# Kernel tuning notes

Hardware: AMD Instinct MI355X
Metric: run time of the kernel (lower is better)

Reference implementation:

```python
import jax, jax.numpy as jnp
import numpy as np

N = 50000          # nodes
E = 800000         # edges (avg degree 16)
FEAT = 128         # self.feat_dim
MAX_SPK = 3
SPK_DIM = 16
SPA_DIM = 16
OUT = 64


def _lin(key, din, dout):
    kw, kb = jax.random.split(key)
    w = jax.random.normal(kw, (din, dout), dtype=jnp.float32) * (1.0 / np.sqrt(din))
    b = jax.random.normal(kb, (dout,), dtype=jnp.float32) * 0.01
    return w, b


def setup_inputs() -> dict:
    key = jax.random.key(0)
    ks = jax.random.split(key, 16)
    D = 7 * FEAT + 5  # 901
    x = jax.random.normal(ks[0], (N, D), dtype=jnp.float32)
    # last column is a speaker count in {1..4} (clamped to max 3 in forward)
    num_spk = jax.random.randint(ks[1], (N,), 1, 5).astype(jnp.float32)
    x = x.at[:, -1].set(num_spk)
    edge_index = jax.random.randint(ks[2], (2, E), 0, N, dtype=jnp.int32)
    edge_attr = jnp.zeros((E,), dtype=jnp.int32)  # all pass the (==111)|(==0) filter

    speaker_w, speaker_b = _lin(ks[3], MAX_SPK, SPK_DIM)
    spatial_w, spatial_b = _lin(ks[4], 4, SPA_DIM)
    # face_trans params
    f1_w, f1_b = _lin(ks[5], FEAT, OUT)
    f2_w, f2_b = _lin(ks[6], FEAT + SPK_DIM + SPA_DIM, OUT)
    fe_w, fe_b = _lin(ks[7], 2 * OUT, 2)
    # face_body_trans params
    g1_w, g1_b = _lin(ks[8], FEAT, OUT)
    g2_w, g2_b = _lin(ks[9], FEAT + SPK_DIM + SPA_DIM, OUT)
    ge_w, ge_b = _lin(ks[10], 2 * OUT, 2)
    return dict(x=x, edge_index=edge_index, edge_attr=edge_attr,
                speaker_w=speaker_w, speaker_b=speaker_b,
                spatial_w=spatial_w, spatial_b=spatial_b,
                f1_w=f1_w, f1_b=f1_b, f2_w=f2_w, f2_b=f2_b, fe_w=fe_w, fe_b=fe_b,
                g1_w=g1_w, g1_b=g1_b, g2_w=g2_w, g2_b=g2_b, ge_w=ge_w, ge_b=ge_b)


def _edge_conv(h, src, dst, valid, ew, eb):
    # PyG EdgeConv (aggr='max'): out_i = max_j MLP([x_i, x_j - x_i])
    hi = h[dst]                                   # [E, 64]
    hj = h[src]                                   # [E, 64]
    msg = jnp.concatenate([hi, hj - hi], axis=1) @ ew + eb  # [E, 2]
    msg = jnp.where(valid[:, None], msg, -jnp.inf)
    out = jax.ops.segment_max(msg, dst, num_segments=h.shape[0])
    return jnp.where(jnp.isfinite(out), out, 0.0)  # empty segments -> 0 (PyG fill)


def reference(x, edge_index, edge_attr,
              speaker_w, speaker_b, spatial_w, spatial_b,
              f1_w, f1_b, f2_w, f2_b, fe_w, fe_b,
              g1_w, g1_b, g2_w, g2_b, ge_w, ge_b):
    valid = (edge_attr == 111) | (edge_attr == 0)
    src, dst = edge_index[0], edge_index[1]

    # speaker-count embedding: one_hot(clamp(x[:,-1]-1, max=2)) -> Linear(3,16)
    spk_idx = jnp.minimum(x[:, -1] - 1.0, MAX_SPK - 1).astype(jnp.int32)
    spk = jax.nn.one_hot(spk_idx, MAX_SPK, dtype=x.dtype) @ speaker_w + speaker_b
    spa = x[:, -5:-1] @ spatial_w + spatial_b

    def block(feat, fc1_w, fc1_b, fc2_w, fc2_b, ew, eb):
        # dropout p=0.9 is identity in eval mode
        h = (feat @ fc1_w + fc1_b) + (jnp.concatenate([feat, spk, spa], axis=1) @ fc2_w + fc2_b)
        return _edge_conv(h, src, dst, valid, ew, eb)

    o_face = block(x[:, :FEAT], f1_w, f1_b, f2_w, f2_b, fe_w, fe_b)
    o_body = block(x[:, FEAT:2 * FEAT], g1_w, g1_b, g2_w, g2_b, ge_w, ge_b)
    return o_face + o_body
```

## Files before the change

kernel.cpp:

```cpp
#include <hip/hip_runtime.h>
#include <hip/hip_bf16.h>
#include <math.h>

#define ROWLEN 901
#define NEGENC 0x007FFFFFu

__device__ __forceinline__ unsigned encf(float f) {
    unsigned u = __float_as_uint(f);
    return (u & 0x80000000u) ? ~u : (u | 0x80000000u);
}
__device__ __forceinline__ float decf(unsigned u) {
    return (u & 0x80000000u) ? __uint_as_float(u ^ 0x80000000u)
                             : __uint_as_float(~u);
}

__global__ __launch_bounds__(256) void k_compose(
    const float* __restrict__ spkw, const float* __restrict__ spkb,
    const float* __restrict__ spaw, const float* __restrict__ spab,
    const float* __restrict__ f1w, const float* __restrict__ f1b,
    const float* __restrict__ f2w, const float* __restrict__ f2b,
    const float* __restrict__ few, const float* __restrict__ feb,
    const float* __restrict__ g1w, const float* __restrict__ g1b,
    const float* __restrict__ g2w, const float* __restrict__ g2b,
    const float* __restrict__ gew, const float* __restrict__ geb,
    float* __restrict__ C, float* __restrict__ Sp,
    float* __restrict__ Tab, float* __restrict__ Cst)
{
    const int t = threadIdx.x;
    __shared__ float sEW[2][256];
    __shared__ float sUV[2][2][2][16][2];
    __shared__ float sBE[8][8];

    sEW[0][t] = few[t];
    sEW[1][t] = gew[t];
    __syncthreads();

    {
        const int blk = t >> 7;
        const int fr  = t & 127;
        const float* w1 = blk ? g1w : f1w;
        const float* w2 = blk ? g2w : f2w;
        const float* e  = sEW[blk];
        float a0 = 0.f, a1 = 0.f, a2 = 0.f, a3 = 0.f;
        #pragma unroll
        for (int k4 = 0; k4 < 16; ++k4) {
            const float4 wa = *(const float4*)(w1 + fr * 64 + k4 * 4);
            const float4 wb = *(const float4*)(w2 + fr * 64 + k4 * 4);
            const float wv[4] = {wa.x + wb.x, wa.y + wb.y, wa.z + wb.z, wa.w + wb.w};
            #pragma unroll
            for (int j = 0; j < 4; ++j) {
                const int k = k4 * 4 + j;
                const float eb0 = e[(64 + k) * 2 + 0];
                const float eb1 = e[(64 + k) * 2 + 1];
                const float ea0 = e[k * 2 + 0] - eb0;
                const float ea1 = e[k * 2 + 1] - eb1;
                a0 += wv[j] * ea0; a1 += wv[j] * ea1;
                a2 += wv[j] * eb0; a3 += wv[j] * eb1;
            }
        }
        C[t * 4 + 0] = a0; C[t * 4 + 1] = a1;
        C[t * 4 + 2] = a2; C[t * 4 + 3] = a3;
    }

    {
        const int c    = t & 1;
        const int k16  = (t >> 1) & 15;
        const int role = (t >> 5) & 1;
        const int blk  = (t >> 6) & 1;
        const int isV  = (t >> 7) & 1;
        const float* w2 = blk ? g2w : f2w;
        const float* e  = sEW[blk];
        const int row = (isV ? 144 : 128) + k16;
        float acc = 0.f;
        #pragma unroll
        for (int k4 = 0; k4 < 16; ++k4) {
            const float4 w = *(const float4*)(w2 + row * 64 + k4 * 4);
            const float wv[4] = {w.x, w.y, w.z, w.w};
            #pragma unroll
            for (int j = 0; j < 4; ++j) {
                const int k = k4 * 4 + j;
                const float ev = role ? e[(64 + k) * 2 + c]
                                      : (e[k * 2 + c] - e[(64 + k) * 2 + c]);
                acc += wv[j] * ev;
            }
        }
        sUV[isV][blk][role][k16][c] = acc;
    }

    if (t < 64) {
        const int combo = t >> 3;
        const int part  = t & 7;
        const int c = combo & 1, role = (combo >> 1) & 1, blk = combo >> 2;
        const float* b1 = blk ? g1b : f1b;
        const float* b2 = blk ? g2b : f2b;
        const float* e  = sEW[blk];
        float acc = 0.f;
        #pragma unroll
        for (int j = 0; j < 8; ++j) {
            const int k = part * 8 + j;
            const float ev = role ? e[(64 + k) * 2 + c]
                                  : (e[k * 2 + c] - e[(64 + k) * 2 + c]);
            acc += (b1[k] + b2[k]) * ev;
        }
        sBE[combo][part] = acc;
    }
    __syncthreads();

    if (t < 24) {
        const int blk = t / 12, rem = t % 12;
        const int idx = rem >> 2, q = rem & 3;
        const int role = q >> 1, c = q & 1;
        float acc = 0.f;
        #pragma unroll
        for (int k = 0; k < 16; ++k)
            acc += spkw[idx * 16 + k] * sUV[0][blk][role][k][c];
        Tab[blk * 12 + idx * 4 + q] = acc;
    } else if (t >= 32 && t < 64) {
        const int u = t - 32;
        const int blk = u >> 4, rem = u & 15;
        const int r = rem >> 2, q = rem & 3;
        const int role = q >> 1, c = q & 1;
        float acc = 0.f;
        #pragma unroll
        for (int k = 0; k < 16; ++k)
            acc += spaw[r * 16 + k] * sUV[1][blk][role][k][c];
        Sp[blk * 16 + r * 4 + q] = acc;
    } else if (t >= 64 && t < 72) {
        const int u = t - 64;
        const int blk = u >> 2, q = u & 3;
        const int role = q >> 1, c = q & 1;
        const float* ebv = blk ? geb : feb;
        float acc = (role == 0) ? ebv[c] : 0.f;
        #pragma unroll
        for (int k = 0; k < 16; ++k) {
            acc += spkb[k] * sUV[0][blk][role][k][c];
            acc += spab[k] * sUV[1][blk][role][k][c];
        }
        #pragma unroll
        for (int p = 0; p < 8; ++p) acc += sBE[u][p];
        Cst[blk * 4 + q] = acc;
    }
}

__global__ __launch_bounds__(256) void k_node(
    const float* __restrict__ x,
    const float* __restrict__ C, const float* __restrict__ Sp,
    const float* __restrict__ Tab, const float* __restrict__ Cst,
    float4* __restrict__ Adat, float4* __restrict__ Bdat,
    unsigned* __restrict__ maxbuf, int* __restrict__ cnt, int nnodes)
{
    const int wave = threadIdx.x >> 6;
    const int lane = threadIdx.x & 63;
    const int node = blockIdx.x * 4 + wave;
    if (node >= nnodes) return;

    const float* xr = x + (size_t)node * ROWLEN;
    const int half = lane >> 5;
    const int l32  = lane & 31;
    const float* xh = xr + half * 128;
    const float4* C4 = (const float4*)C;

    float xs0 = 0.f, xs1 = 0.f, xs2 = 0.f, xs3 = 0.f, xspk = 0.f;
    if (lane == 0) {
        xs0 = xr[896]; xs1 = xr[897]; xs2 = xr[898]; xs3 = xr[899];
        xspk = xr[900];
    }

    float a0 = 0.f, a1 = 0.f, a2 = 0.f, a3 = 0.f;
    #pragma unroll
    for (int k = 0; k < 4; ++k) {
        const int el = l32 + 32 * k;
        const float v = xh[el];
        const float4 cr = C4[half * 128 + el];
        a0 += v * cr.x; a1 += v * cr.y; a2 += v * cr.z; a3 += v * cr.w;
    }

    #pragma unroll
    for (int m = 16; m >= 1; m >>= 1) {
        a0 += __shfl_xor(a0, m, 64);
        a1 += __shfl_xor(a1, m, 64);
        a2 += __shfl_xor(a2, m, 64);
        a3 += __shfl_xor(a3, m, 64);
    }
    const float b0 = __shfl(a0, 32, 64);
    const float b1 = __shfl(a1, 32, 64);
    const float b2 = __shfl(a2, 32, 64);
    const float b3 = __shfl(a3, 32, 64);

    if (lane == 0) {
        const float xs[4] = {xs0, xs1, xs2, xs3};
        int idx = (int)fminf(xspk - 1.0f, 2.0f);
        idx = idx < 0 ? 0 : (idx > 2 ? 2 : idx);

        const float pq[2][4] = {{a0, a1, a2, a3}, {b0, b1, b2, b3}};
        float av[4], bv[4];
        #pragma unroll
        for (int blk = 0; blk < 2; ++blk) {
            #pragma unroll
            for (int c = 0; c < 2; ++c) {
                float ea = Tab[blk * 12 + idx * 4 + c] + Cst[blk * 4 + c];
                float eb = Tab[blk * 12 + idx * 4 + 2 + c] + Cst[blk * 4 + 2 + c];
                #pragma unroll
                for (int r = 0; r < 4; ++r) {
                    ea += xs[r] * Sp[blk * 16 + r * 4 + c];
                    eb += xs[r] * Sp[blk * 16 + r * 4 + 2 + c];
                }
                av[blk * 2 + c] = pq[blk][c] + ea;
                bv[blk * 2 + c] = pq[blk][2 + c] + eb;
            }
        }
        Adat[node] = make_float4(av[0], av[1], av[2], av[3]);
        Bdat[node] = make_float4(bv[0], bv[1], bv[2], bv[3]);
        *(uint4*)(maxbuf + (size_t)node * 4) =
            make_uint4(NEGENC, NEGENC, NEGENC, NEGENC);
        cnt[node] = 0;
    }
}

__global__ __launch_bounds__(256) void k_scatter(
    const int* __restrict__ ei, const int* __restrict__ ea,
    const float4* __restrict__ Bdat,
    int* __restrict__ cnt, int* __restrict__ bucket,
    unsigned* __restrict__ maxbuf, int nedges, int cap)
{
    const int e = blockIdx.x * blockDim.x + threadIdx.x;
    if (e >= nedges) return;
    const int attr = ea[e];
    if (!(attr == 0 || attr == 111)) return;
    const int s = ei[e];
    const int d = ei[nedges + e];
    const int pos = atomicAdd(cnt + d, 1);
    if (pos < cap) {
        bucket[(size_t)d * cap + pos] = s;
    } else {
        const float4 b = Bdat[s];
        unsigned* mb = maxbuf + (size_t)d * 4;
        atomicMax(mb + 0, encf(b.x));
        atomicMax(mb + 1, encf(b.y));
        atomicMax(mb + 2, encf(b.z));
        atomicMax(mb + 3, encf(b.w));
    }
}

__global__ __launch_bounds__(256) void k_gather(
    const float4* __restrict__ Adat, const float4* __restrict__ Bdat,
    const int* __restrict__ cnt, const int* __restrict__ bucket,
    const unsigned* __restrict__ maxbuf,
    float* __restrict__ out, int nnodes, int cap)
{
    const int t = blockIdx.x * blockDim.x + threadIdx.x;
    const int n = t >> 2, sub = t & 3;
    if (n >= nnodes) return;
    int c = cnt[n]; if (c > cap) c = cap;

    float m0 = -INFINITY, m1 = -INFINITY, m2 = -INFINITY, m3 = -INFINITY;
    const int* row = bucket + (size_t)n * cap;
    for (int i = sub; i < c; i += 4) {
        const int s = row[i];
        const float4 b = Bdat[s];
        m0 = fmaxf(m0, b.x); m1 = fmaxf(m1, b.y);
        m2 = fmaxf(m2, b.z); m3 = fmaxf(m3, b.w);
    }
    #pragma unroll
    for (int msk = 1; msk <= 2; msk <<= 1) {
        m0 = fmaxf(m0, __shfl_xor(m0, msk, 64));
        m1 = fmaxf(m1, __shfl_xor(m1, msk, 64));
        m2 = fmaxf(m2, __shfl_xor(m2, msk, 64));
        m3 = fmaxf(m3, __shfl_xor(m3, msk, 64));
    }
    if (sub == 0) {
        const uint4 ov = *(const uint4*)(maxbuf + (size_t)n * 4);
        m0 = fmaxf(m0, decf(ov.x)); m1 = fmaxf(m1, decf(ov.y));
        m2 = fmaxf(m2, decf(ov.z)); m3 = fmaxf(m3, decf(ov.w));
        const float4 a = Adat[n];
        const float f0 = isfinite(m0) ? a.x + m0 : 0.f;
        const float f1 = isfinite(m1) ? a.y + m1 : 0.f;
        const float f2 = isfinite(m2) ? a.z + m2 : 0.f;
        const float f3 = isfinite(m3) ? a.w + m3 : 0.f;
        out[(size_t)n * 2 + 0] = f0 + f2;
        out[(size_t)n * 2 + 1] = f1 + f3;
    }
}

extern "C" void kernel_launch(void* const* d_in, const int* in_sizes, int n_in,
                              void* d_out, int out_size, void* d_ws, size_t ws_size,
                              hipStream_t stream) {
    const float* x    = (const float*)d_in[0];
    const int*   ei   = (const int*)d_in[1];
    const int*   ea   = (const int*)d_in[2];
    const float* spkw = (const float*)d_in[3];
    const float* spkb = (const float*)d_in[4];
    const float* spaw = (const float*)d_in[5];
    const float* spab = (const float*)d_in[6];
    const float* f1w  = (const float*)d_in[7];
    const float* f1b  = (const float*)d_in[8];
    const float* f2w  = (const float*)d_in[9];
    const float* f2b  = (const float*)d_in[10];
    const float* few  = (const float*)d_in[11];
    const float* feb  = (const float*)d_in[12];
    const float* g1w  = (const float*)d_in[13];
    const float* g1b  = (const float*)d_in[14];
    const float* g2w  = (const float*)d_in[15];
    const float* g2b  = (const float*)d_in[16];
    const float* gew  = (const float*)d_in[17];
    const float* geb  = (const float*)d_in[18];

    const int N = in_sizes[0] / ROWLEN;
    const int E = in_sizes[2];

    char* ws = (char*)d_ws;
    float*    C      = (float*)(ws + 0);
    float*    Sp     = (float*)(ws + 4096);
    float*    Tab    = (float*)(ws + 4096 + 128);
    float*    Cst    = (float*)(ws + 4096 + 256);
    size_t off = 16384;
    float4*   Adat   = (float4*)(ws + off);   off += (size_t)N * 16;
    float4*   Bdat   = (float4*)(ws + off);   off += (size_t)N * 16;
    unsigned* maxbuf = (unsigned*)(ws + off); off += (size_t)N * 16;
    int*      cnt    = (int*)(ws + off);      off += (((size_t)N * 4 + 255) / 256) * 256;
    int*      bucket = (int*)(ws + off);
    const size_t remain = ws_size > off ? ws_size - off : 0;
    size_t cap_sz = remain / ((size_t)N * 4);
    int CAP = cap_sz > 64 ? 64 : (int)cap_sz;

    k_compose<<<1, 256, 0, stream>>>(spkw, spkb, spaw, spab,
                                     f1w, f1b, f2w, f2b, few, feb,
                                     g1w, g1b, g2w, g2b, gew, geb,
                                     C, Sp, Tab, Cst);

    k_node<<<(N + 3) / 4, 256, 0, stream>>>(x, C, Sp, Tab, Cst,
                                            Adat, Bdat, maxbuf, cnt, N);

    k_scatter<<<(E + 255) / 256, 256, 0, stream>>>(ei, ea, Bdat, cnt, bucket,
                                                   maxbuf, E, CAP);

    k_gather<<<((size_t)N * 4 + 255) / 256, 256, 0, stream>>>(Adat, Bdat, cnt, bucket,
                                                              maxbuf, (float*)d_out, N, CAP);
}
```

Measured before the change: 331.4 us.

## Parallelize weight composition across blocks, pad edge counters, prefetch bucket indices

The C-matrix composition previously done by one 256-thread block is split across 16 extra blocks, with each row reduced by 16 lanes through shuffles. The remaining block still computes the other small tables. The per-node edge counters are padded to a stride of 8 ints to spread atomic contention across cache lines. The gather loop also software-prefetches the next bucket index. The cost is more workspace for the counters and a slightly larger launch.

```diff
diff --git a/kernel.cpp b/kernel.cpp
--- a/kernel.cpp
+++ b/kernel.cpp
@@ -4,6 +4,7 @@
 
 #define ROWLEN 901
 #define NEGENC 0x007FFFFFu
+#define CNTSTRIDE 8
 
 __device__ __forceinline__ unsigned encf(float f) {
     unsigned u = __float_as_uint(f);
@@ -27,6 +28,45 @@
     float* __restrict__ Tab, float* __restrict__ Cst)
 {
     const int t = threadIdx.x;
+
+    if (blockIdx.x < 16) {
+        const int row = blockIdx.x * 16 + (t >> 4);
+        const int kk  = t & 15;
+        const int blk = row >> 7;
+        const int fr  = row & 127;
+        const float* w1 = blk ? g1w : f1w;
+        const float* w2 = blk ? g2w : f2w;
+        const float* e  = blk ? gew : few;
+
+        const float4 wa = *(const float4*)(w1 + fr * 64 + kk * 4);
+        const float4 wb = *(const float4*)(w2 + fr * 64 + kk * 4);
+        const float wv[4] = {wa.x + wb.x, wa.y + wb.y, wa.z + wb.z, wa.w + wb.w};
+
+        float a0 = 0.f, a1 = 0.f, a2 = 0.f, a3 = 0.f;
+        #pragma unroll
+        for (int j = 0; j < 4; ++j) {
+            const int k = kk * 4 + j;
+            const float eb0 = e[(64 + k) * 2 + 0];
+            const float eb1 = e[(64 + k) * 2 + 1];
+            const float ea0 = e[k * 2 + 0] - eb0;
+            const float ea1 = e[k * 2 + 1] - eb1;
+            a0 += wv[j] * ea0; a1 += wv[j] * ea1;
+            a2 += wv[j] * eb0; a3 += wv[j] * eb1;
+        }
+        #pragma unroll
+        for (int m = 1; m <= 8; m <<= 1) {
+            a0 += __shfl_xor(a0, m, 64);
+            a1 += __shfl_xor(a1, m, 64);
+            a2 += __shfl_xor(a2, m, 64);
+            a3 += __shfl_xor(a3, m, 64);
+        }
+        if (kk == 0) {
+            C[row * 4 + 0] = a0; C[row * 4 + 1] = a1;
+            C[row * 4 + 2] = a2; C[row * 4 + 3] = a3;
+        }
+        return;
+    }
+
     __shared__ float sEW[2][256];
     __shared__ float sUV[2][2][2][16][2];
     __shared__ float sBE[8][8];
@@ -34,33 +74,6 @@
     sEW[0][t] = few[t];
     sEW[1][t] = gew[t];
     __syncthreads();
-
-    {
-        const int blk = t >> 7;
-        const int fr  = t & 127;
-        const float* w1 = blk ? g1w : f1w;
-        const float* w2 = blk ? g2w : f2w;
-        const float* e  = sEW[blk];
-        float a0 = 0.f, a1 = 0.f, a2 = 0.f, a3 = 0.f;
-        #pragma unroll
-        for (int k4 = 0; k4 < 16; ++k4) {
-            const float4 wa = *(const float4*)(w1 + fr * 64 + k4 * 4);
-            const float4 wb = *(const float4*)(w2 + fr * 64 + k4 * 4);
-            const float wv[4] = {wa.x + wb.x, wa.y + wb.y, wa.z + wb.z, wa.w + wb.w};
-            #pragma unroll
-            for (int j = 0; j < 4; ++j) {
-                const int k = k4 * 4 + j;
-                const float eb0 = e[(64 + k) * 2 + 0];
-                const float eb1 = e[(64 + k) * 2 + 1];
-                const float ea0 = e[k * 2 + 0] - eb0;
-                const float ea1 = e[k * 2 + 1] - eb1;
-                a0 += wv[j] * ea0; a1 += wv[j] * ea1;
-                a2 += wv[j] * eb0; a3 += wv[j] * eb1;
-            }
-        }
-        C[t * 4 + 0] = a0; C[t * 4 + 1] = a1;
-        C[t * 4 + 2] = a2; C[t * 4 + 3] = a3;
-    }
 
     {
         const int c    = t & 1;
@@ -213,7 +226,7 @@
         Bdat[node] = make_float4(bv[0], bv[1], bv[2], bv[3]);
         *(uint4*)(maxbuf + (size_t)node * 4) =
             make_uint4(NEGENC, NEGENC, NEGENC, NEGENC);
-        cnt[node] = 0;
+        cnt[(size_t)node * CNTSTRIDE] = 0;
     }
 }
 
@@ -229,7 +242,7 @@
     if (!(attr == 0 || attr == 111)) return;
     const int s = ei[e];
     const int d = ei[nedges + e];
-    const int pos = atomicAdd(cnt + d, 1);
+    const int pos = atomicAdd(cnt + (size_t)d * CNTSTRIDE, 1);
     if (pos < cap) {
         bucket[(size_t)d * cap + pos] = s;
     } else {
@@ -251,12 +264,16 @@
     const int t = blockIdx.x * blockDim.x + threadIdx.x;
     const int n = t >> 2, sub = t & 3;
     if (n >= nnodes) return;
-    int c = cnt[n]; if (c > cap) c = cap;
+    int c = cnt[(size_t)n * CNTSTRIDE]; if (c > cap) c = cap;
 
     float m0 = -INFINITY, m1 = -INFINITY, m2 = -INFINITY, m3 = -INFINITY;
     const int* row = bucket + (size_t)n * cap;
-    for (int i = sub; i < c; i += 4) {
-        const int s = row[i];
+    int i = sub;
+    int s_next = (i < c) ? row[i] : 0;
+    while (i < c) {
+        const int s = s_next;
+        i += 4;
+        if (i < c) s_next = row[i];
         const float4 b = Bdat[s];
         m0 = fmaxf(m0, b.x); m1 = fmaxf(m1, b.y);
         m2 = fmaxf(m2, b.z); m3 = fmaxf(m3, b.w);
@@ -317,16 +334,16 @@
     float4*   Adat   = (float4*)(ws + off);   off += (size_t)N * 16;
     float4*   Bdat   = (float4*)(ws + off);   off += (size_t)N * 16;
     unsigned* maxbuf = (unsigned*)(ws + off); off += (size_t)N * 16;
-    int*      cnt    = (int*)(ws + off);      off += (((size_t)N * 4 + 255) / 256) * 256;
+    int*      cnt    = (int*)(ws + off);      off += (((size_t)N * CNTSTRIDE * 4 + 255) / 256) * 256;
     int*      bucket = (int*)(ws + off);
     const size_t remain = ws_size > off ? ws_size - off : 0;
     size_t cap_sz = remain / ((size_t)N * 4);
     int CAP = cap_sz > 64 ? 64 : (int)cap_sz;
 
-    k_compose<<<1, 256, 0, stream>>>(spkw, spkb, spaw, spab,
-                                     f1w, f1b, f2w, f2b, few, feb,
-                                     g1w, g1b, g2w, g2b, gew, geb,
-                                     C, Sp, Tab, Cst);
+    k_compose<<<17, 256, 0, stream>>>(spkw, spkb, spaw, spab,
+                                      f1w, f1b, f2w, f2b, few, feb,
+                                      g1w, g1b, g2w, g2b, gew, geb,
+                                      C, Sp, Tab, Cst);
 
     k_node<<<(N + 3) / 4, 256, 0, stream>>>(x, C, Sp, Tab, Cst,
                                             Adat, Bdat, maxbuf, cnt, N);
```

Result: faster. 321.5 us (-3.0%).
